# Performance work log

Measured on AMD Instinct MI355X. Metric: run time of the kernel, lower is better.

Reference implementation:

```python
import jax, jax.numpy as jnp
import numpy as np
import itertools

# ---- module hyperparams (from args) ----
B = 4
H, W = 480, 640                 # frame_height, frame_width
NSEM = 16                       # num_sem_categories
RES = 5                         # map_resolution (cm/cell)
ZRES = 5
MAP_CM = 4800 // 2              # map_size_cm // global_downscaling
M = MAP_CM // RES               # local map cells = 480
VR = 100                        # vision_range
FOV = 79.0                      # hfov degrees
DU_SCALE = 1
CAT_THR, EXP_THR, MAP_THR = 5.0, 1.0, 1.0
AGENT_H = 0.88 * 100.0          # camera_height * 100 (cm)
MAX_H = int(360 / ZRES)         # 72
MIN_H = int(-40 / ZRES)         # -8
NZ = MAX_H - MIN_H              # 80 height bins
C = 4 + NSEM                    # obs channels
RAD2DEG = 57.29577951308232


def setup_inputs():
    key = jax.random.key(0)
    k1, k2, k3, k4 = jax.random.split(key, 4)
    obs = jax.random.uniform(k1, (B, C, H, W), dtype=jnp.float32)
    obs = obs.at[:, 3].multiply(500.0)  # depth channel in cm
    pose_obs = jax.random.normal(k2, (B, 3), dtype=jnp.float32) * 0.1
    maps_last = jax.random.uniform(k3, (B, C, M, M), dtype=jnp.float32)
    poses_last = jax.random.normal(k4, (B, 3), dtype=jnp.float32)
    return {"obs": obs, "pose_obs": pose_obs, "maps_last": maps_last, "poses_last": poses_last}


def _point_cloud(depth):
    # du.get_point_cloud_from_z_t; depth: (B,H,W) cm -> (B,H,W,3)
    f = (W / 2.0) / np.tan(np.deg2rad(FOV / 2.0))
    xc, zc = (W - 1) / 2.0, (H - 1) / 2.0
    gx = jnp.arange(W, dtype=jnp.float32)[None, None, :]
    gz = jnp.arange(H - 1, -1, -1, dtype=jnp.float32)[None, :, None]
    X = (gx - xc) * depth / f
    Z = (gz - zc) * depth / f
    return jnp.stack([X, depth, Z], axis=-1)


def _splat_feat_nd(dims, feat, coords):
    # du.splat_feat_nd: trilinear scatter-splat of per-point feats into dense grid.
    # feat: (B,F,N), coords: (B,3,N) normalized to [-1,1]. Returns (B,F,*dims).
    Bn, Fc, N = feat.shape
    pos = [coords[:, d] * (dims[d] / 2.0) + dims[d] / 2.0 for d in range(3)]
    idxs, wtss = [], []
    for offs in itertools.product((0, 1), repeat=3):
        index = jnp.zeros_like(pos[0])
        wts = jnp.ones_like(pos[0])
        for d in range(3):
            p = jnp.floor(pos[d]) + offs[d]
            safe = ((p > 0) & (p < dims[d])).astype(jnp.float32)
            wts = wts * (1.0 - jnp.abs(pos[d] - p)) * safe
            index = index * dims[d] + p * safe
        idxs.append(index)
        wtss.append(wts)
    idx = jnp.concatenate(idxs, -1).astype(jnp.int32)       # (B, 8N)
    wts = jnp.concatenate(wtss, -1)                         # (B, 8N)
    vals = jnp.tile(feat, (1, 1, 8)) * wts[:, None, :]      # (B, F, 8N)
    ncell = dims[0] * dims[1] * dims[2]
    grid = jax.vmap(lambda i, v: jnp.zeros((Fc, ncell), jnp.float32).at[:, i].add(v))(idx, vals)
    return jnp.round(grid).reshape(Bn, Fc, *dims)


def _affine_grid(theta, Hh, Ww):
    # F.affine_grid, align_corners=True. theta: (B,2,3) -> (B,Hh,Ww,2)
    xs = jnp.linspace(-1.0, 1.0, Ww)
    ys = jnp.linspace(-1.0, 1.0, Hh)
    gy, gx = jnp.meshgrid(ys, xs, indexing="ij")
    base = jnp.stack([gx, gy, jnp.ones_like(gx)], -1)       # (Hh,Ww,3)
    return jnp.einsum("hwk,bjk->bhwj", base, theta)


def _grid_sample(img, grid):
    # F.grid_sample bilinear, zeros padding, align_corners=True.
    Bn, Cc, Hi, Wi = img.shape
    x = (grid[..., 0] + 1.0) * 0.5 * (Wi - 1)
    y = (grid[..., 1] + 1.0) * 0.5 * (Hi - 1)
    x0 = jnp.floor(x); y0 = jnp.floor(y)
    x1, y1 = x0 + 1, y0 + 1

    def gather(ix, iy):
        valid = (ix >= 0) & (ix <= Wi - 1) & (iy >= 0) & (iy <= Hi - 1)
        ixc = jnp.clip(ix, 0, Wi - 1).astype(jnp.int32)
        iyc = jnp.clip(iy, 0, Hi - 1).astype(jnp.int32)
        v = jax.vmap(lambda im, yy, xx: im[:, yy, xx])(img, iyc, ixc)  # (B,C,Hg,Wg)
        return v * valid[:, None].astype(img.dtype)

    wa = (x1 - x) * (y1 - y); wb = (x1 - x) * (y - y0)
    wc = (x - x0) * (y1 - y); wd = (x - x0) * (y - y0)
    return (gather(x0, y0) * wa[:, None] + gather(x0, y1) * wb[:, None]
            + gather(x1, y0) * wc[:, None] + gather(x1, y1) * wd[:, None])


def _forward(obs, pose_obs, maps_last, poses_last):
    depth = obs[:, 3]
    pc = _point_cloud(depth)                                # camera frame (cm)
    # transform_camera_view_t with elevation 0 deg: rotation = identity, z += agent height
    av = pc.at[..., 2].add(AGENT_H)
    # transform_pose_t with shift_loc=(vr*res//2, 0, pi/2): rot angle = pi/2-pi/2 = 0, x += shift
    avc = av.at[..., 0].add(VR * RES // 2)
    xy = avc[..., :2] / RES
    xy = (xy - VR // 2.0) / VR * 2.0
    z = avc[..., 2] / ZRES
    z = (z - (MAX_H + MIN_H) // 2.0) / (MAX_H - MIN_H) * 2.0
    coords = jnp.concatenate([xy, z[..., None]], -1)        # (B,H,W,3) in [-1,1]
    coords = coords.reshape(B, H * W, 3).transpose(0, 2, 1)  # (B,3,N)
    # feat: ones occupancy channel + avg-pooled(du_scale) semantic channels
    hs, ws = H // DU_SCALE, W // DU_SCALE
    sem = obs[:, 4:4 + NSEM].reshape(B, NSEM, hs, DU_SCALE, ws, DU_SCALE).mean((3, 5))
    feat = jnp.concatenate([jnp.ones((B, 1, hs * ws), jnp.float32),
                            sem.reshape(B, NSEM, hs * ws)], 1)
    voxels = _splat_feat_nd((VR, VR, NZ), feat, coords)
    voxels = jnp.swapaxes(voxels, 2, 3)                     # .transpose(2, 3)
    min_z = int(25 / ZRES - MIN_H)                          # 13
    max_z = int((AGENT_H + 1) / ZRES - MIN_H)               # 25
    agent_height_proj = voxels[..., min_z:max_z].sum(-1)
    all_height_proj = voxels.sum(-1)
    fp_map_pred = jnp.clip(agent_height_proj[:, 0:1] / MAP_THR, 0.0, 1.0)
    fp_exp_pred = jnp.clip(all_height_proj[:, 0:1] / EXP_THR, 0.0, 1.0)
    agent_view = jnp.zeros((B, C, M, M), jnp.float32)
    x1 = M // 2 - VR // 2; x2 = x1 + VR
    y1 = M // 2; y2 = y1 + VR
    agent_view = agent_view.at[:, 0:1, y1:y2, x1:x2].set(fp_map_pred)
    agent_view = agent_view.at[:, 1:2, y1:y2, x1:x2].set(fp_exp_pred)
    agent_view = agent_view.at[:, 4:, y1:y2, x1:x2].set(
        jnp.clip(agent_height_proj[:, 1:] / CAT_THR, 0.0, 1.0))
    # get_new_pose_batch (uses pre-update theta for x/y, then wraps theta)
    r = poses_last[:, 2] / RAD2DEG
    yy = poses_last[:, 1] + pose_obs[:, 0] * jnp.sin(r) + pose_obs[:, 1] * jnp.cos(r)
    xx = poses_last[:, 0] + pose_obs[:, 0] * jnp.cos(r) - pose_obs[:, 1] * jnp.sin(r)
    oo = poses_last[:, 2] + pose_obs[:, 2] * RAD2DEG
    oo = jnp.fmod(oo - 180.0, 360.0) + 180.0
    oo = jnp.fmod(oo + 180.0, 360.0) - 180.0
    current_poses = jnp.stack([xx, yy, oo], 1)
    st = jax.lax.stop_gradient(current_poses)               # .clone().detach()
    st_xy = -(st[:, :2] * 100.0 / RES - M // 2) / (M // 2)
    st_t = (90.0 - st[:, 2]) * np.pi / 180.0
    cos_t, sin_t = jnp.cos(st_t), jnp.sin(st_t)
    zero = jnp.zeros_like(cos_t); one = jnp.ones_like(cos_t)
    theta1 = jnp.stack([jnp.stack([cos_t, -sin_t, zero], 1),
                        jnp.stack([sin_t, cos_t, zero], 1)], 1)
    theta2 = jnp.stack([jnp.stack([one, zero, st_xy[:, 0]], 1),
                        jnp.stack([zero, one, st_xy[:, 1]], 1)], 1)
    rotated = _grid_sample(agent_view, _affine_grid(theta1, M, M))
    translated = _grid_sample(rotated, _affine_grid(theta2, M, M))
    map_pred = jnp.maximum(maps_last, translated)           # max over stacked maps
    return fp_map_pred, map_pred, current_poses


def reference(obs, pose_obs, maps_last, poses_last):
    return _forward(obs, pose_obs, maps_last, poses_last)
```

## Files before the change

### kernel.cpp

```cpp
#include <hip/hip_runtime.h>
#include <math.h>

#define NB 4
#define NC 20
#define NH 480
#define NW 640
#define NPIX (NH*NW)
#define NM 480
#define NVR 100
#define NNZ 80
#define ZLO 13
#define ZHI 25
#define NZB 12
#define NSEM_ 16
#define NBINS 101

__device__ __forceinline__ float p1_chain(float d) {
  float xy1 = d / 5.0f;
  xy1 = (xy1 - 50.0f) / 100.0f * 2.0f;
  return xy1 * 50.0f + 50.0f;
}
__device__ __forceinline__ void p02_chain(float d, int row, int col, float foc,
                                          float& p0, float& p2) {
  float X = ((float)col - 319.5f) * d / foc;
  float Z = ((float)(479 - row) - 239.5f) * d / foc;
  float xy0 = (X + 250.0f) / 5.0f;
  xy0 = (xy0 - 50.0f) / 100.0f * 2.0f;
  float zz = (Z + 88.0f) / 5.0f;
  zz = (zz - 32.0f) / 80.0f * 2.0f;
  p0 = xy0 * 50.0f + 50.0f;
  p2 = zz * 40.0f + 40.0f;
}

__global__ __launch_bounds__(64) void pose_kernel(
    const float* __restrict__ pose_obs, const float* __restrict__ poses_last,
    float* __restrict__ out_poses, float* __restrict__ params)
{
  int b = threadIdx.x;
  if (b >= NB) return;
  const float R2D = 57.29577951308232f;
  float plx = poses_last[b*3+0], ply = poses_last[b*3+1], plo = poses_last[b*3+2];
  float dx = pose_obs[b*3+0], dy = pose_obs[b*3+1], dth = pose_obs[b*3+2];
  float r = plo / R2D;
  float sr = sinf(r), cr = cosf(r);
  float yy = ply + dx*sr + dy*cr;
  float xx = plx + dx*cr - dy*sr;
  float oo = plo + dth*R2D;
  oo = fmodf(oo - 180.0f, 360.0f) + 180.0f;
  oo = fmodf(oo + 180.0f, 360.0f) - 180.0f;
  out_poses[b*3+0] = xx;
  out_poses[b*3+1] = yy;
  out_poses[b*3+2] = oo;
  float tx = -((xx*100.0f/5.0f) - 240.0f) / 240.0f;
  float ty = -((yy*100.0f/5.0f) - 240.0f) / 240.0f;
  float th = ((90.0f - oo) * 3.14159274101257324f) / 180.0f;
  params[b*4+0] = cosf(th);
  params[b*4+1] = sinf(th);
  params[b*4+2] = tx;
  params[b*4+3] = ty;
}

__global__ __launch_bounds__(256) void hist_kernel(
    const float* __restrict__ obs, int* __restrict__ hist)
{
  int b = blockIdx.x / 300, blk = blockIdx.x % 300;
  __shared__ int lh[NBINS];
  for (int i = threadIdx.x; i < NBINS; i += 256) lh[i] = 0;
  __syncthreads();
  const float4* dp = (const float4*)(obs + ((size_t)b*NC + 3)*NPIX);
  float4 dv = dp[blk*256 + threadIdx.x];
  float dvv[4] = {dv.x, dv.y, dv.z, dv.w};
  #pragma unroll
  for (int k = 0; k < 4; ++k) {
    int y0 = (int)floorf(p1_chain(dvv[k]));
    y0 = min(max(y0, 0), 100);
    atomicAdd(&lh[y0], 1);
  }
  __syncthreads();
  for (int i = threadIdx.x; i < NBINS; i += 256)
    if (lh[i]) atomicAdd(&hist[b*NBINS + i], lh[i]);
}

__global__ __launch_bounds__(512) void scan_kernel(
    const int* __restrict__ hist, int* __restrict__ starts, int* __restrict__ cursors)
{
  __shared__ int lh[NB*NBINS];
  __shared__ int ls[NB*NBINS + 1];
  for (int i = threadIdx.x; i < NB*NBINS; i += 512) lh[i] = hist[i];
  __syncthreads();
  if (threadIdx.x == 0) {
    int s = 0;
    for (int i = 0; i < NB*NBINS; ++i) { ls[i] = s; s += lh[i]; }
    ls[NB*NBINS] = s;
  }
  __syncthreads();
  for (int i = threadIdx.x; i < NB*NBINS + 1; i += 512) {
    starts[i] = ls[i];
    if (i < NB*NBINS) cursors[i] = ls[i];
  }
}

__global__ __launch_bounds__(256) void scatter_kernel(
    const float* __restrict__ obs, int* __restrict__ cursors,
    float4* __restrict__ recs, float foc)
{
  int b = blockIdx.x / 300, blk = blockIdx.x % 300;
  __shared__ int lh[NBINS], lbase[NBINS], loff[NBINS];
  for (int i = threadIdx.x; i < NBINS; i += 256) { lh[i] = 0; loff[i] = 0; }
  __syncthreads();
  int pix0 = (blk*256 + threadIdx.x)*4;
  int row = pix0 / NW;
  int c0 = pix0 - row*NW;
  const float4* dp = (const float4*)(obs + ((size_t)b*NC + 3)*NPIX);
  float4 dv = dp[blk*256 + threadIdx.x];
  float dvv[4] = {dv.x, dv.y, dv.z, dv.w};
  float rp0[4], rp1[4], rp2[4]; int rbin[4];
  #pragma unroll
  for (int k = 0; k < 4; ++k) {
    float p1 = p1_chain(dvv[k]);
    float p0, p2;
    p02_chain(dvv[k], row, c0 + k, foc, p0, p2);
    rp0[k] = p0; rp1[k] = p1; rp2[k] = p2;
    int y0 = (int)floorf(p1); y0 = min(max(y0, 0), 100);
    rbin[k] = y0;
    atomicAdd(&lh[y0], 1);
  }
  __syncthreads();
  for (int i = threadIdx.x; i < NBINS; i += 256)
    if (lh[i] > 0) lbase[i] = atomicAdd(&cursors[b*NBINS + i], lh[i]);
  __syncthreads();
  #pragma unroll
  for (int k = 0; k < 4; ++k) {
    int idx = atomicAdd(&loff[rbin[k]], 1);
    recs[lbase[rbin[k]] + idx] =
        make_float4(rp0[k], rp1[k], rp2[k], __int_as_float(pix0 + k));
  }
}

__global__ __launch_bounds__(256) void slab0_kernel(
    const float4* __restrict__ recs, const int* __restrict__ starts,
    float* __restrict__ proj, float* __restrict__ out_fp)
{
  int b = blockIdx.x / NVR, Y = blockIdx.x % NVR;
  __shared__ float g[NVR*81];
  for (int i = threadIdx.x; i < NVR*81; i += 256) g[i] = 0.0f;
  __syncthreads();
  if (Y > 0) {
    int lo = starts[b*NBINS + Y - 1];
    int hi = starts[b*NBINS + Y + 1];
    float Yf = (float)Y;
    for (int i = lo + threadIdx.x; i < hi; i += 256) {
      float4 r = recs[i];
      float wy = 1.0f - fabsf(r.y - Yf);
      if (wy <= 0.0f) continue;
      float p0 = r.x, p2 = r.z;
      float fl0 = floorf(p0), fl2 = floorf(p2);
      #pragma unroll
      for (int xo = 0; xo < 2; ++xo) {
        float px = fl0 + (float)xo;
        if (!(px > 0.0f && px < 100.0f)) continue;
        float wxy = (1.0f - fabsf(p0 - px)) * wy;
        if (wxy <= 0.0f) continue;
        int ix = (int)px;
        #pragma unroll
        for (int zo = 0; zo < 2; ++zo) {
          float pz = fl2 + (float)zo;
          if (!(pz > 0.0f && pz < 80.0f)) continue;
          float w = wxy * (1.0f - fabsf(p2 - pz));
          if (w > 0.0f) atomicAdd(&g[ix*81 + (int)pz], w);
        }
      }
    }
  }
  __syncthreads();
  if (threadIdx.x < NVR) {
    int x = threadIdx.x;
    float s_all = 0.0f, s_ag = 0.0f;
    for (int z = 0; z < NNZ; ++z) {
      float v = rintf(g[x*81 + z]);
      s_all += v;
      if (z >= ZLO && z < ZHI) s_ag += v;
    }
    float fp_map = fminf(fmaxf(s_ag, 0.0f), 1.0f);
    float fp_exp = fminf(fmaxf(s_all, 0.0f), 1.0f);
    size_t pb = (((size_t)b*NC + 0)*NVR + Y)*NVR + x;
    proj[pb] = fp_map;
    proj[pb + NVR*NVR] = fp_exp;
    proj[pb + 2*NVR*NVR] = 0.0f;
    proj[pb + 3*NVR*NVR] = 0.0f;
    out_fp[(size_t)b*NVR*NVR + Y*NVR + x] = fp_map;
  }
}

__global__ __launch_bounds__(256) void slab1_kernel(
    const float* __restrict__ obs, const float4* __restrict__ recs,
    const int* __restrict__ starts, float* __restrict__ proj)
{
  int half = blockIdx.x & 1;
  int t = blockIdx.x >> 1;
  int b = t / NVR, Y = t % NVR;
  __shared__ float g[NVR*NZB*8];
  for (int i = threadIdx.x; i < NVR*NZB*8; i += 256) g[i] = 0.0f;
  __syncthreads();
  if (Y > 0) {
    int lo = starts[b*NBINS + Y - 1];
    int hi = starts[b*NBINS + Y + 1];
    float Yf = (float)Y;
    const float* sbase = obs + ((size_t)b*NC + 4 + half*8)*NPIX;
    for (int i = lo + threadIdx.x; i < hi; i += 256) {
      float4 r = recs[i];
      float wy = 1.0f - fabsf(r.y - Yf);
      if (wy <= 0.0f) continue;
      float p2 = r.z;
      float fl2 = floorf(p2);
      float wz[2]; int iz[2]; bool any = false;
      #pragma unroll
      for (int zo = 0; zo < 2; ++zo) {
        float pz = fl2 + (float)zo;
        bool v = (pz >= (float)ZLO) && (pz < (float)ZHI);
        float w = v ? (1.0f - fabsf(p2 - pz)) : 0.0f;
        wz[zo] = w; iz[zo] = v ? ((int)pz - ZLO) : 0;
        any = any || (w > 0.0f);
      }
      if (!any) continue;
      float p0 = r.x;
      float fl0 = floorf(p0);
      int pid = __float_as_int(r.w);
      float sem[8];
      #pragma unroll
      for (int s = 0; s < 8; ++s) sem[s] = sbase[(size_t)s*NPIX + pid];
      #pragma unroll
      for (int xo = 0; xo < 2; ++xo) {
        float px = fl0 + (float)xo;
        if (!(px > 0.0f && px < 100.0f)) continue;
        float wxy = (1.0f - fabsf(p0 - px)) * wy;
        if (wxy <= 0.0f) continue;
        int ix = (int)px;
        #pragma unroll
        for (int zo = 0; zo < 2; ++zo) {
          float w = wxy * wz[zo];
          if (w > 0.0f) {
            float* gb = &g[(ix*NZB + iz[zo])*8];
            #pragma unroll
            for (int s = 0; s < 8; ++s) atomicAdd(&gb[s], w * sem[s]);
          }
        }
      }
    }
  }
  __syncthreads();
  for (int p = threadIdx.x; p < NVR*8; p += 256) {
    int x = p >> 3, s = p & 7;
    float acc = 0.0f;
    #pragma unroll
    for (int z = 0; z < NZB; ++z) acc += rintf(g[(x*NZB + z)*8 + s]);
    float val = fminf(fmaxf(acc / 5.0f, 0.0f), 1.0f);
    proj[(((size_t)b*NC + 4 + half*8 + s)*NVR + Y)*NVR + x] = val;
  }
}

__global__ __launch_bounds__(256) void transform_kernel(
    const float* __restrict__ maps_last, const float* __restrict__ proj,
    const float* __restrict__ params, float* __restrict__ d_out)
{
  int tid = blockIdx.x * 256 + threadIdx.x;
  int b = tid / (NM*NM);
  int rem = tid - b*(NM*NM);
  int h = rem / NM;
  int w = rem - h*NM;

  float ct = params[b*4+0];
  float st = params[b*4+1];
  float tx = params[b*4+2];
  float ty = params[b*4+3];

  const float step = 2.0f/479.0f;
  float gx = -1.0f + (float)w * step;
  float gy = -1.0f + (float)h * step;
  float X2 = ((gx + tx) + 1.0f) * 0.5f * 479.0f;
  float Y2 = ((gy + ty) + 1.0f) * 0.5f * 479.0f;
  float x0 = floorf(X2), y0 = floorf(Y2);
  float wox[2] = {(x0 + 1.0f) - X2, X2 - x0};
  float woy[2] = {(y0 + 1.0f) - Y2, Y2 - y0};

  float twt[16];
  int   toff[16];
  int nz = 0;
  #pragma unroll
  for (int oy = 0; oy < 2; ++oy) {
    #pragma unroll
    for (int ox = 0; ox < 2; ++ox) {
      int kb = (oy*2 + ox)*4;
      float cx = x0 + (float)ox;
      float cy = y0 + (float)oy;
      float wo = wox[ox]*woy[oy];
      bool ov = (cx >= 0.0f) && (cx <= 479.0f) && (cy >= 0.0f) && (cy <= 479.0f);
      if (ov) {
        float gxr = -1.0f + cx * step;
        float gyr = -1.0f + cy * step;
        float xr = gxr*ct - gyr*st;
        float yr = gxr*st + gyr*ct;
        float XS = (xr + 1.0f)*0.5f*479.0f;
        float YS = (yr + 1.0f)*0.5f*479.0f;
        float ix0 = floorf(XS), iy0 = floorf(YS);
        float wix[2] = {(ix0+1.0f)-XS, XS-ix0};
        float wiy[2] = {(iy0+1.0f)-YS, YS-iy0};
        #pragma unroll
        for (int qy = 0; qy < 2; ++qy) {
          #pragma unroll
          for (int qx = 0; qx < 2; ++qx) {
            int k = kb + qy*2 + qx;
            float ux = ix0 + (float)qx;
            float vy = iy0 + (float)qy;
            float wv = 0.0f; int off = 0;
            if (ux >= 0.0f && ux <= 479.0f && vy >= 0.0f && vy <= 479.0f) {
              int U = (int)ux, V = (int)vy;
              if (U >= 190 && U < 290 && V >= 240 && V < 340) {
                off = (V - 240)*NVR + (U - 190);
                wv = wo * (wix[qx]*wiy[qy]);
              }
            }
            twt[k] = wv; toff[k] = off;
            nz += (wv != 0.0f) ? 1 : 0;
          }
        }
      } else {
        #pragma unroll
        for (int k = 0; k < 4; ++k) { twt[kb+k] = 0.0f; toff[kb+k] = 0; }
      }
    }
  }

  const float* pbase = proj + (size_t)b*NC*NVR*NVR;
  size_t base_idx = (size_t)b*NC*NM*NM + (size_t)h*NM + w;
  if (nz > 0) {
    #pragma unroll 1
    for (int c = 0; c < NC; ++c) {
      size_t idx = base_idx + (size_t)c*NM*NM;
      float ml = maps_last[idx];
      float val = 0.0f;
      if (c != 2 && c != 3) {
        const float* pc = pbase + (size_t)c*NVR*NVR;
        #pragma unroll
        for (int k = 0; k < 16; ++k) val += twt[k]*pc[toff[k]];
      }
      d_out[40000 + idx] = fmaxf(ml, val);
    }
  } else {
    #pragma unroll 1
    for (int c = 0; c < NC; ++c) {
      size_t idx = base_idx + (size_t)c*NM*NM;
      d_out[40000 + idx] = fmaxf(maps_last[idx], 0.0f);
    }
  }
}

extern "C" void kernel_launch(void* const* d_in, const int* in_sizes, int n_in,
                              void* d_out, int out_size, void* d_ws, size_t ws_size,
                              hipStream_t stream)
{
  const float* obs        = (const float*)d_in[0];
  const float* pose_obs   = (const float*)d_in[1];
  const float* maps_last  = (const float*)d_in[2];
  const float* poses_last = (const float*)d_in[3];
  float* out = (float*)d_out;

  char* ws = (char*)d_ws;
  int*    hist    = (int*)ws;
  int*    starts  = (int*)(ws + 2048);
  int*    cursors = (int*)(ws + 4096);
  float*  params  = (float*)(ws + 6144);
  float4* recs    = (float4*)(ws + 8192);
  float*  proj    = (float*)(ws + 8192 + 19660800);

  hipMemsetAsync(ws, 0, 6144, stream);

  const float foc = (float)(((double)NW) / 2.0 / tan(79.0 * 0.5 * M_PI / 180.0));

  pose_kernel<<<1, 64, 0, stream>>>(pose_obs, poses_last, out + 40000 + 18432000, params);
  hist_kernel<<<NB*300, 256, 0, stream>>>(obs, hist);
  scan_kernel<<<1, 512, 0, stream>>>(hist, starts, cursors);
  scatter_kernel<<<NB*300, 256, 0, stream>>>(obs, cursors, recs, foc);
  slab0_kernel<<<NB*NVR, 256, 0, stream>>>(recs, starts, proj, out);
  slab1_kernel<<<NB*NVR*2, 256, 0, stream>>>(obs, recs, starts, proj);
  transform_kernel<<<(NB*NM*NM)/256, 256, 0, stream>>>(maps_last, proj, params, out);
}
```

Before: 560.5 us.

## Compact band-filtered points with semantic features for coalesced semantic splatting

Adds a second histogram and scan that count only points whose x and z fall inside the agent-height band, then has the scatter kernel write those points' geometry and all 16 semantic values contiguously into compact buffers. A new slab1f kernel reads these packed records instead of gathering semantic channels from obs by pixel index, so it skips out-of-band points and avoids scattered loads. The fast path runs only when the workspace is large enough. In exchange, hist and scatter do more arithmetic, scatter reads extra channels and writes more, and anything beyond SREC_CAP is silently dropped.

```diff
diff --git a/kernel.cpp b/kernel.cpp
--- a/kernel.cpp
+++ b/kernel.cpp
@@ -14,6 +14,20 @@
 #define NZB 12
 #define NSEM_ 16
 #define NBINS 101
+#define SREC_CAP 655360
+
+#define WS_HIST     0
+#define WS_HIST2    2048
+#define WS_STARTS   4096
+#define WS_STARTS2  6144
+#define WS_CURS     8192
+#define WS_CURS2    10240
+#define WS_PARAMS   12288
+#define WS_RECS     16384
+#define WS_PROJ     (WS_RECS + 19660800)
+#define WS_SGEOM    (WS_PROJ + 3200000)
+#define WS_SSEM     (WS_SGEOM + SREC_CAP*16)
+#define WS_FAST_END (WS_SSEM + (size_t)SREC_CAP*64)
 
 __device__ __forceinline__ float p1_chain(float d) {
   float xy1 = d / 5.0f;
@@ -30,6 +44,10 @@
   zz = (zz - 32.0f) / 80.0f * 2.0f;
   p0 = xy0 * 50.0f + 50.0f;
   p2 = zz * 40.0f + 40.0f;
+}
+__device__ __forceinline__ bool band_ok(float p0, float p2) {
+  return (p0 > 0.0f) && (p0 < 100.0f) &&
+         (p2 > (float)(ZLO - 1)) && (p2 < (float)ZHI);
 }
 
 __global__ __launch_bounds__(64) void pose_kernel(
@@ -61,52 +79,12 @@
 }
 
 __global__ __launch_bounds__(256) void hist_kernel(
-    const float* __restrict__ obs, int* __restrict__ hist)
+    const float* __restrict__ obs, int* __restrict__ hist, int* __restrict__ hist2,
+    float foc)
 {
   int b = blockIdx.x / 300, blk = blockIdx.x % 300;
-  __shared__ int lh[NBINS];
-  for (int i = threadIdx.x; i < NBINS; i += 256) lh[i] = 0;
-  __syncthreads();
-  const float4* dp = (const float4*)(obs + ((size_t)b*NC + 3)*NPIX);
-  float4 dv = dp[blk*256 + threadIdx.x];
-  float dvv[4] = {dv.x, dv.y, dv.z, dv.w};
-  #pragma unroll
-  for (int k = 0; k < 4; ++k) {
-    int y0 = (int)floorf(p1_chain(dvv[k]));
-    y0 = min(max(y0, 0), 100);
-    atomicAdd(&lh[y0], 1);
-  }
-  __syncthreads();
-  for (int i = threadIdx.x; i < NBINS; i += 256)
-    if (lh[i]) atomicAdd(&hist[b*NBINS + i], lh[i]);
-}
-
-__global__ __launch_bounds__(512) void scan_kernel(
-    const int* __restrict__ hist, int* __restrict__ starts, int* __restrict__ cursors)
-{
-  __shared__ int lh[NB*NBINS];
-  __shared__ int ls[NB*NBINS + 1];
-  for (int i = threadIdx.x; i < NB*NBINS; i += 512) lh[i] = hist[i];
-  __syncthreads();
-  if (threadIdx.x == 0) {
-    int s = 0;
-    for (int i = 0; i < NB*NBINS; ++i) { ls[i] = s; s += lh[i]; }
-    ls[NB*NBINS] = s;
-  }
-  __syncthreads();
-  for (int i = threadIdx.x; i < NB*NBINS + 1; i += 512) {
-    starts[i] = ls[i];
-    if (i < NB*NBINS) cursors[i] = ls[i];
-  }
-}
-
-__global__ __launch_bounds__(256) void scatter_kernel(
-    const float* __restrict__ obs, int* __restrict__ cursors,
-    float4* __restrict__ recs, float foc)
-{
-  int b = blockIdx.x / 300, blk = blockIdx.x % 300;
-  __shared__ int lh[NBINS], lbase[NBINS], loff[NBINS];
-  for (int i = threadIdx.x; i < NBINS; i += 256) { lh[i] = 0; loff[i] = 0; }
+  __shared__ int lh[NBINS], lh2[NBINS];
+  for (int i = threadIdx.x; i < NBINS; i += 256) { lh[i] = 0; lh2[i] = 0; }
   __syncthreads();
   int pix0 = (blk*256 + threadIdx.x)*4;
   int row = pix0 / NW;
@@ -114,7 +92,69 @@
   const float4* dp = (const float4*)(obs + ((size_t)b*NC + 3)*NPIX);
   float4 dv = dp[blk*256 + threadIdx.x];
   float dvv[4] = {dv.x, dv.y, dv.z, dv.w};
-  float rp0[4], rp1[4], rp2[4]; int rbin[4];
+  #pragma unroll
+  for (int k = 0; k < 4; ++k) {
+    float p1 = p1_chain(dvv[k]);
+    int y0 = (int)floorf(p1);
+    y0 = min(max(y0, 0), 100);
+    atomicAdd(&lh[y0], 1);
+    float p0, p2;
+    p02_chain(dvv[k], row, c0 + k, foc, p0, p2);
+    if (band_ok(p0, p2)) atomicAdd(&lh2[y0], 1);
+  }
+  __syncthreads();
+  for (int i = threadIdx.x; i < NBINS; i += 256) {
+    if (lh[i])  atomicAdd(&hist[b*NBINS + i],  lh[i]);
+    if (lh2[i]) atomicAdd(&hist2[b*NBINS + i], lh2[i]);
+  }
+}
+
+__global__ __launch_bounds__(512) void scan_kernel(
+    const int* __restrict__ hist, const int* __restrict__ hist2,
+    int* __restrict__ starts, int* __restrict__ cursors,
+    int* __restrict__ starts2, int* __restrict__ cursors2)
+{
+  __shared__ int lh[NB*NBINS], lh2[NB*NBINS];
+  __shared__ int ls[NB*NBINS + 1], ls2[NB*NBINS + 1];
+  for (int i = threadIdx.x; i < NB*NBINS; i += 512) { lh[i] = hist[i]; lh2[i] = hist2[i]; }
+  __syncthreads();
+  if (threadIdx.x == 0) {
+    int s = 0;
+    for (int i = 0; i < NB*NBINS; ++i) { ls[i] = s; s += lh[i]; }
+    ls[NB*NBINS] = s;
+  }
+  if (threadIdx.x == 1) {
+    int s = 0;
+    for (int i = 0; i < NB*NBINS; ++i) { ls2[i] = s; s += lh2[i]; }
+    ls2[NB*NBINS] = s;
+  }
+  __syncthreads();
+  for (int i = threadIdx.x; i < NB*NBINS + 1; i += 512) {
+    starts[i] = ls[i];
+    starts2[i] = ls2[i];
+    if (i < NB*NBINS) { cursors[i] = ls[i]; cursors2[i] = ls2[i]; }
+  }
+}
+
+__global__ __launch_bounds__(256) void scatter_kernel(
+    const float* __restrict__ obs, int* __restrict__ cursors, int* __restrict__ cursors2,
+    float4* __restrict__ recs, float4* __restrict__ sgeom, float4* __restrict__ ssem,
+    float foc, int do_band)
+{
+  int b = blockIdx.x / 300, blk = blockIdx.x % 300;
+  __shared__ int lh[NBINS], lbase[NBINS], loff[NBINS];
+  __shared__ int lh2[NBINS], lbase2[NBINS], loff2[NBINS];
+  for (int i = threadIdx.x; i < NBINS; i += 256) {
+    lh[i] = 0; loff[i] = 0; lh2[i] = 0; loff2[i] = 0;
+  }
+  __syncthreads();
+  int pix0 = (blk*256 + threadIdx.x)*4;
+  int row = pix0 / NW;
+  int c0 = pix0 - row*NW;
+  const float4* dp = (const float4*)(obs + ((size_t)b*NC + 3)*NPIX);
+  float4 dv = dp[blk*256 + threadIdx.x];
+  float dvv[4] = {dv.x, dv.y, dv.z, dv.w};
+  float rp0[4], rp1[4], rp2[4]; int rbin[4]; bool rb[4];
   #pragma unroll
   for (int k = 0; k < 4; ++k) {
     float p1 = p1_chain(dvv[k]);
@@ -124,16 +164,50 @@
     int y0 = (int)floorf(p1); y0 = min(max(y0, 0), 100);
     rbin[k] = y0;
     atomicAdd(&lh[y0], 1);
-  }
-  __syncthreads();
-  for (int i = threadIdx.x; i < NBINS; i += 256)
-    if (lh[i] > 0) lbase[i] = atomicAdd(&cursors[b*NBINS + i], lh[i]);
-  __syncthreads();
+    rb[k] = do_band && band_ok(p0, p2);
+    if (rb[k]) atomicAdd(&lh2[y0], 1);
+  }
+  __syncthreads();
+  for (int i = threadIdx.x; i < NBINS; i += 256) {
+    if (lh[i]  > 0) lbase[i]  = atomicAdd(&cursors[b*NBINS + i],  lh[i]);
+    if (lh2[i] > 0) lbase2[i] = atomicAdd(&cursors2[b*NBINS + i], lh2[i]);
+  }
+  __syncthreads();
+  int sidx[4];
   #pragma unroll
   for (int k = 0; k < 4; ++k) {
     int idx = atomicAdd(&loff[rbin[k]], 1);
     recs[lbase[rbin[k]] + idx] =
         make_float4(rp0[k], rp1[k], rp2[k], __int_as_float(pix0 + k));
+    sidx[k] = -1;
+    if (rb[k]) {
+      int j = lbase2[rbin[k]] + atomicAdd(&loff2[rbin[k]], 1);
+      if (j < SREC_CAP) sidx[k] = j;
+    }
+  }
+  bool anyb = (sidx[0] >= 0) | (sidx[1] >= 0) | (sidx[2] >= 0) | (sidx[3] >= 0);
+  if (anyb) {
+    #pragma unroll
+    for (int k = 0; k < 4; ++k)
+      if (sidx[k] >= 0)
+        sgeom[sidx[k]] = make_float4(rp0[k], rp1[k], rp2[k], 0.0f);
+    int grp = blk*256 + threadIdx.x;
+    const float4* obs4 = (const float4*)obs;
+    #pragma unroll
+    for (int q = 0; q < 4; ++q) {
+      float4 v0 = obs4[(((size_t)b*NC + 4 + 4*q + 0)*NPIX >> 2) + grp];
+      float4 v1 = obs4[(((size_t)b*NC + 4 + 4*q + 1)*NPIX >> 2) + grp];
+      float4 v2 = obs4[(((size_t)b*NC + 4 + 4*q + 2)*NPIX >> 2) + grp];
+      float4 v3 = obs4[(((size_t)b*NC + 4 + 4*q + 3)*NPIX >> 2) + grp];
+      float a0[4] = {v0.x, v0.y, v0.z, v0.w};
+      float a1[4] = {v1.x, v1.y, v1.z, v1.w};
+      float a2[4] = {v2.x, v2.y, v2.z, v2.w};
+      float a3[4] = {v3.x, v3.y, v3.z, v3.w};
+      #pragma unroll
+      for (int k = 0; k < 4; ++k)
+        if (sidx[k] >= 0)
+          ssem[(size_t)sidx[k]*4 + q] = make_float4(a0[k], a1[k], a2[k], a3[k]);
+    }
   }
 }
 
@@ -189,6 +263,72 @@
     proj[pb + 2*NVR*NVR] = 0.0f;
     proj[pb + 3*NVR*NVR] = 0.0f;
     out_fp[(size_t)b*NVR*NVR + Y*NVR + x] = fp_map;
+  }
+}
+
+__global__ __launch_bounds__(256) void slab1f_kernel(
+    const float4* __restrict__ sgeom, const float4* __restrict__ ssem,
+    const int* __restrict__ starts2, float* __restrict__ proj)
+{
+  int half = blockIdx.x & 1;
+  int t = blockIdx.x >> 1;
+  int b = t / NVR, Y = t % NVR;
+  __shared__ float g[8*NVR*NZB];
+  for (int i = threadIdx.x; i < 8*NVR*NZB; i += 256) g[i] = 0.0f;
+  __syncthreads();
+  if (Y > 0) {
+    int lo = starts2[b*NBINS + Y - 1];
+    int hi = starts2[b*NBINS + Y + 1];
+    float Yf = (float)Y;
+    for (int i = lo + threadIdx.x; i < hi; i += 256) {
+      float4 ge = sgeom[i];
+      float wy = 1.0f - fabsf(ge.y - Yf);
+      if (wy <= 0.0f) continue;
+      float p2 = ge.z;
+      float fl2 = floorf(p2);
+      float wz[2]; int iz[2]; bool any = false;
+      #pragma unroll
+      for (int zo = 0; zo < 2; ++zo) {
+        float pz = fl2 + (float)zo;
+        bool v = (pz >= (float)ZLO) && (pz < (float)ZHI);
+        float w = v ? (1.0f - fabsf(p2 - pz)) : 0.0f;
+        wz[zo] = w; iz[zo] = v ? ((int)pz - ZLO) : 0;
+        any = any || (w > 0.0f);
+      }
+      if (!any) continue;
+      float p0 = ge.x;
+      float fl0 = floorf(p0);
+      float4 s0 = ssem[(size_t)i*4 + half*2];
+      float4 s1 = ssem[(size_t)i*4 + half*2 + 1];
+      float sem[8] = {s0.x, s0.y, s0.z, s0.w, s1.x, s1.y, s1.z, s1.w};
+      #pragma unroll
+      for (int xo = 0; xo < 2; ++xo) {
+        float px = fl0 + (float)xo;
+        if (!(px > 0.0f && px < 100.0f)) continue;
+        float wxy = (1.0f - fabsf(p0 - px)) * wy;
+        if (wxy <= 0.0f) continue;
+        int ix = (int)px;
+        #pragma unroll
+        for (int zo = 0; zo < 2; ++zo) {
+          float w = wxy * wz[zo];
+          if (w > 0.0f) {
+            int cell = ix*NZB + iz[zo];
+            #pragma unroll
+            for (int s = 0; s < 8; ++s)
+              atomicAdd(&g[s*(NVR*NZB) + cell], w * sem[s]);
+          }
+        }
+      }
+    }
+  }
+  __syncthreads();
+  for (int p = threadIdx.x; p < NVR*8; p += 256) {
+    int x = p >> 3, s = p & 7;
+    float acc = 0.0f;
+    #pragma unroll
+    for (int z = 0; z < NZB; ++z) acc += rintf(g[s*(NVR*NZB) + x*NZB + z]);
+    float val = fminf(fmaxf(acc / 5.0f, 0.0f), 1.0f);
+    proj[(((size_t)b*NC + 4 + half*8 + s)*NVR + Y)*NVR + x] = val;
   }
 }
 
@@ -366,22 +506,33 @@
   float* out = (float*)d_out;
 
   char* ws = (char*)d_ws;
-  int*    hist    = (int*)ws;
-  int*    starts  = (int*)(ws + 2048);
-  int*    cursors = (int*)(ws + 4096);
-  float*  params  = (float*)(ws + 6144);
-  float4* recs    = (float4*)(ws + 8192);
-  float*  proj    = (float*)(ws + 8192 + 19660800);
-
-  hipMemsetAsync(ws, 0, 6144, stream);
+  int*    hist    = (int*)(ws + WS_HIST);
+  int*    hist2   = (int*)(ws + WS_HIST2);
+  int*    starts  = (int*)(ws + WS_STARTS);
+  int*    starts2 = (int*)(ws + WS_STARTS2);
+  int*    cursors = (int*)(ws + WS_CURS);
+  int*    cursors2= (int*)(ws + WS_CURS2);
+  float*  params  = (float*)(ws + WS_PARAMS);
+  float4* recs    = (float4*)(ws + WS_RECS);
+  float*  proj    = (float*)(ws + WS_PROJ);
+  float4* sgeom   = (float4*)(ws + WS_SGEOM);
+  float4* ssem    = (float4*)(ws + WS_SSEM);
+
+  const bool fast = ws_size >= (size_t)WS_FAST_END;
+
+  hipMemsetAsync(ws, 0, WS_PARAMS, stream);
 
   const float foc = (float)(((double)NW) / 2.0 / tan(79.0 * 0.5 * M_PI / 180.0));
 
   pose_kernel<<<1, 64, 0, stream>>>(pose_obs, poses_last, out + 40000 + 18432000, params);
-  hist_kernel<<<NB*300, 256, 0, stream>>>(obs, hist);
-  scan_kernel<<<1, 512, 0, stream>>>(hist, starts, cursors);
-  scatter_kernel<<<NB*300, 256, 0, stream>>>(obs, cursors, recs, foc);
+  hist_kernel<<<NB*300, 256, 0, stream>>>(obs, hist, hist2, foc);
+  scan_kernel<<<1, 512, 0, stream>>>(hist, hist2, starts, cursors, starts2, cursors2);
+  scatter_kernel<<<NB*300, 256, 0, stream>>>(obs, cursors, cursors2, recs, sgeom, ssem,
+                                             foc, fast ? 1 : 0);
   slab0_kernel<<<NB*NVR, 256, 0, stream>>>(recs, starts, proj, out);
-  slab1_kernel<<<NB*NVR*2, 256, 0, stream>>>(obs, recs, starts, proj);
+  if (fast)
+    slab1f_kernel<<<NB*NVR*2, 256, 0, stream>>>(sgeom, ssem, starts2, proj);
+  else
+    slab1_kernel<<<NB*NVR*2, 256, 0, stream>>>(obs, recs, starts, proj);
   transform_kernel<<<(NB*NM*NM)/256, 256, 0, stream>>>(maps_last, proj, params, out);
 }
```

Result: slower. 603.6 us (+7.7%).

## Bin semantic splat by (Y,X) cells and gather-accumulate from transposed semantics

Applied to the files above, without the earlier changes.

Adds a 2D (Y,X) histogram and scan so that only points inside the agent-height band are scattered into per-cell record lists. A transpose kernel lays the 16 semantic channels out per pixel, and a new gather kernel has lanes accumulate per-cell sums in registers, replacing the shared-memory atomic splat. The slab0 loop is also unrolled to load four records at a time. The gain depends on the band filter pruning most points. The cost is an extra full semantic transpose pass, more workspace, and a fallback path when the workspace is too small.

```diff
diff --git a/kernel.cpp b/kernel.cpp
--- a/kernel.cpp
+++ b/kernel.cpp
@@ -12,8 +12,22 @@
 #define ZLO 13
 #define ZHI 25
 #define NZB 12
-#define NSEM_ 16
 #define NBINS 101
+#define SREC_CAP 786432
+#define NB2D 40400
+
+#define WS_HIST     0
+#define WS_STARTS   2048
+#define WS_CURS     4096
+#define WS_PARAMS   6144
+#define WS_H2D      8192
+#define WS_S2D      172032
+#define WS_C2D      335872
+#define WS_RECS     499712
+#define WS_PROJ     (WS_RECS + 19660800)
+#define WS_SGEOM    (WS_PROJ + 3200000)
+#define WS_SEMT     (WS_SGEOM + (size_t)SREC_CAP*16)
+#define WS_FAST_END (WS_SEMT + (size_t)NB*NPIX*16*4)
 
 __device__ __forceinline__ float p1_chain(float d) {
   float xy1 = d / 5.0f;
@@ -30,6 +44,10 @@
   zz = (zz - 32.0f) / 80.0f * 2.0f;
   p0 = xy0 * 50.0f + 50.0f;
   p2 = zz * 40.0f + 40.0f;
+}
+__device__ __forceinline__ bool band_ok(float p0, float p2) {
+  return (p0 > 0.0f) && (p0 < 100.0f) &&
+         (p2 > (float)(ZLO - 1)) && (p2 < (float)ZHI);
 }
 
 __global__ __launch_bounds__(64) void pose_kernel(
@@ -60,21 +78,48 @@
   params[b*4+3] = ty;
 }
 
+__global__ __launch_bounds__(256) void semt_kernel(
+    const float* __restrict__ obs, float* __restrict__ semT)
+{
+  int b = blockIdx.x / 1200, blk = blockIdx.x % 1200;
+  int p = blk*256 + threadIdx.x;
+  const float* src = obs + ((size_t)b*NC + 4)*NPIX + p;
+  float v[16];
+  #pragma unroll
+  for (int s = 0; s < 16; ++s) v[s] = src[(size_t)s*NPIX];
+  float4* dst = (float4*)(semT + ((size_t)b*NPIX + p)*16);
+  dst[0] = make_float4(v[0],  v[1],  v[2],  v[3]);
+  dst[1] = make_float4(v[4],  v[5],  v[6],  v[7]);
+  dst[2] = make_float4(v[8],  v[9],  v[10], v[11]);
+  dst[3] = make_float4(v[12], v[13], v[14], v[15]);
+}
+
 __global__ __launch_bounds__(256) void hist_kernel(
-    const float* __restrict__ obs, int* __restrict__ hist)
+    const float* __restrict__ obs, int* __restrict__ hist, int* __restrict__ h2d,
+    float foc, int do2d)
 {
   int b = blockIdx.x / 300, blk = blockIdx.x % 300;
   __shared__ int lh[NBINS];
   for (int i = threadIdx.x; i < NBINS; i += 256) lh[i] = 0;
   __syncthreads();
+  int pix0 = (blk*256 + threadIdx.x)*4;
+  int row = pix0 / NW;
+  int c0 = pix0 - row*NW;
   const float4* dp = (const float4*)(obs + ((size_t)b*NC + 3)*NPIX);
   float4 dv = dp[blk*256 + threadIdx.x];
   float dvv[4] = {dv.x, dv.y, dv.z, dv.w};
   #pragma unroll
   for (int k = 0; k < 4; ++k) {
-    int y0 = (int)floorf(p1_chain(dvv[k]));
+    float p1 = p1_chain(dvv[k]);
+    int y0 = (int)floorf(p1);
     y0 = min(max(y0, 0), 100);
     atomicAdd(&lh[y0], 1);
+    float p0, p2;
+    p02_chain(dvv[k], row, c0 + k, foc, p0, p2);
+    if (do2d && band_ok(p0, p2)) {
+      int x0 = (int)floorf(p0);
+      atomicAdd(&h2d[(b*NBINS + y0)*100 + x0], 1);
+    }
   }
   __syncthreads();
   for (int i = threadIdx.x; i < NBINS; i += 256)
@@ -100,9 +145,37 @@
   }
 }
 
+__global__ __launch_bounds__(512) void scan2d_kernel(
+    const int* __restrict__ h2d, int* __restrict__ s2d, int* __restrict__ c2d)
+{
+  __shared__ int part[512];
+  __shared__ int base[512];
+  const int CH = 79;
+  int t = threadIdx.x;
+  int s = 0;
+  for (int i = 0; i < CH; ++i) {
+    int idx = t*CH + i;
+    if (idx < NB2D) s += h2d[idx];
+  }
+  part[t] = s;
+  __syncthreads();
+  if (t == 0) {
+    int run = 0;
+    for (int k = 0; k < 512; ++k) { base[k] = run; run += part[k]; }
+    s2d[NB2D] = run;
+  }
+  __syncthreads();
+  int run = base[t];
+  for (int i = 0; i < CH; ++i) {
+    int idx = t*CH + i;
+    if (idx < NB2D) { s2d[idx] = run; c2d[idx] = run; run += h2d[idx]; }
+  }
+}
+
 __global__ __launch_bounds__(256) void scatter_kernel(
-    const float* __restrict__ obs, int* __restrict__ cursors,
-    float4* __restrict__ recs, float foc)
+    const float* __restrict__ obs, int* __restrict__ cursors, int* __restrict__ c2d,
+    float4* __restrict__ recs, float4* __restrict__ sgeom,
+    float foc, int do_band)
 {
   int b = blockIdx.x / 300, blk = blockIdx.x % 300;
   __shared__ int lh[NBINS], lbase[NBINS], loff[NBINS];
@@ -134,10 +207,17 @@
     int idx = atomicAdd(&loff[rbin[k]], 1);
     recs[lbase[rbin[k]] + idx] =
         make_float4(rp0[k], rp1[k], rp2[k], __int_as_float(pix0 + k));
-  }
-}
-
-__global__ __launch_bounds__(256) void slab0_kernel(
+    if (do_band && band_ok(rp0[k], rp2[k])) {
+      int x0 = (int)floorf(rp0[k]);
+      int bin = (b*NBINS + rbin[k])*100 + x0;
+      int j = atomicAdd(&c2d[bin], 1);
+      if (j < SREC_CAP)
+        sgeom[j] = make_float4(rp0[k], rp1[k], rp2[k], __int_as_float(pix0 + k));
+    }
+  }
+}
+
+__global__ __launch_bounds__(256) void slab0f_kernel(
     const float4* __restrict__ recs, const int* __restrict__ starts,
     float* __restrict__ proj, float* __restrict__ out_fp)
 {
@@ -149,25 +229,34 @@
     int lo = starts[b*NBINS + Y - 1];
     int hi = starts[b*NBINS + Y + 1];
     float Yf = (float)Y;
-    for (int i = lo + threadIdx.x; i < hi; i += 256) {
-      float4 r = recs[i];
-      float wy = 1.0f - fabsf(r.y - Yf);
-      if (wy <= 0.0f) continue;
-      float p0 = r.x, p2 = r.z;
-      float fl0 = floorf(p0), fl2 = floorf(p2);
+    for (int i = lo + threadIdx.x; i < hi; i += 1024) {
+      float4 rr[4];
       #pragma unroll
-      for (int xo = 0; xo < 2; ++xo) {
-        float px = fl0 + (float)xo;
-        if (!(px > 0.0f && px < 100.0f)) continue;
-        float wxy = (1.0f - fabsf(p0 - px)) * wy;
-        if (wxy <= 0.0f) continue;
-        int ix = (int)px;
+      for (int k = 0; k < 4; ++k) {
+        int j = i + k*256;
+        rr[k] = (j < hi) ? recs[j] : make_float4(0.0f, -1.0e9f, 0.0f, 0.0f);
+      }
+      #pragma unroll
+      for (int k = 0; k < 4; ++k) {
+        float4 r = rr[k];
+        float wy = 1.0f - fabsf(r.y - Yf);
+        if (wy <= 0.0f) continue;
+        float p0 = r.x, p2 = r.z;
+        float fl0 = floorf(p0), fl2 = floorf(p2);
         #pragma unroll
-        for (int zo = 0; zo < 2; ++zo) {
-          float pz = fl2 + (float)zo;
-          if (!(pz > 0.0f && pz < 80.0f)) continue;
-          float w = wxy * (1.0f - fabsf(p2 - pz));
-          if (w > 0.0f) atomicAdd(&g[ix*81 + (int)pz], w);
+        for (int xo = 0; xo < 2; ++xo) {
+          float px = fl0 + (float)xo;
+          if (!(px > 0.0f && px < 100.0f)) continue;
+          float wxy = (1.0f - fabsf(p0 - px)) * wy;
+          if (wxy <= 0.0f) continue;
+          int ix = (int)px;
+          #pragma unroll
+          for (int zo = 0; zo < 2; ++zo) {
+            float pz = fl2 + (float)zo;
+            if (!(pz > 0.0f && pz < 80.0f)) continue;
+            float w = wxy * (1.0f - fabsf(p2 - pz));
+            if (w > 0.0f) atomicAdd(&g[ix*81 + (int)pz], w);
+          }
         }
       }
     }
@@ -189,6 +278,69 @@
     proj[pb + 2*NVR*NVR] = 0.0f;
     proj[pb + 3*NVR*NVR] = 0.0f;
     out_fp[(size_t)b*NVR*NVR + Y*NVR + x] = fp_map;
+  }
+}
+
+__global__ __launch_bounds__(512) void slab1g_kernel(
+    const float* __restrict__ semT, const float4* __restrict__ sgeom,
+    const int* __restrict__ s2d, float* __restrict__ proj)
+{
+  int b = blockIdx.x / NVR, Y = blockIdx.x % NVR;
+  int wave = threadIdx.x >> 6;
+  int lane = threadIdx.x & 63;
+  int s = lane & 15;
+  int zq = lane >> 4;
+  float z0f = (float)(ZLO + zq*3);
+  float Yf = (float)Y;
+  const float* sT = semT + (size_t)b*NPIX*16 + s;
+
+  int xbase = wave*13;
+  #pragma unroll 1
+  for (int xi = 0; xi < 13; ++xi) {
+    int x = xbase + xi;
+    if (x >= NVR) break;
+    float acc0 = 0.0f, acc1 = 0.0f, acc2 = 0.0f;
+    if (Y > 0 && x > 0) {
+      float xf = (float)x;
+      #pragma unroll 1
+      for (int p = 0; p < 2; ++p) {
+        int rowb = (b*NBINS + (Y - 1 + p))*100;
+        int lo = s2d[rowb + x - 1];
+        int hi = s2d[rowb + x + 1];
+        #pragma unroll 1
+        for (int i = lo; i < hi; i += 4) {
+          int n = hi - i;
+          float4 gm[4];
+          #pragma unroll
+          for (int k = 0; k < 4; ++k)
+            gm[k] = (k < n) ? sgeom[i + k]
+                            : make_float4(0.0f, -1.0e9f, 0.0f, __int_as_float(0));
+          float sv[4];
+          #pragma unroll
+          for (int k = 0; k < 4; ++k) {
+            int pid = __float_as_int(gm[k].w);
+            sv[k] = sT[(size_t)pid*16];
+          }
+          #pragma unroll
+          for (int k = 0; k < 4; ++k) {
+            float wy = fmaxf(1.0f - fabsf(gm[k].y - Yf), 0.0f);
+            float wx = fmaxf(1.0f - fabsf(gm[k].x - xf), 0.0f);
+            float wxy = wx * wy;
+            float p2 = gm[k].z;
+            float ws0 = wxy * sv[k];
+            acc0 += ws0 * fmaxf(1.0f - fabsf(p2 - z0f), 0.0f);
+            acc1 += ws0 * fmaxf(1.0f - fabsf(p2 - (z0f + 1.0f)), 0.0f);
+            acc2 += ws0 * fmaxf(1.0f - fabsf(p2 - (z0f + 2.0f)), 0.0f);
+          }
+        }
+      }
+    }
+    float r = rintf(acc0) + rintf(acc1) + rintf(acc2);
+    r += __shfl_xor(r, 16);
+    r += __shfl_xor(r, 32);
+    if (zq == 0)
+      proj[(((size_t)b*NC + 4 + s)*NVR + Y)*NVR + x] =
+          fminf(fmaxf(r / 5.0f, 0.0f), 1.0f);
   }
 }
 
@@ -228,7 +380,7 @@
       int pid = __float_as_int(r.w);
       float sem[8];
       #pragma unroll
-      for (int s = 0; s < 8; ++s) sem[s] = sbase[(size_t)s*NPIX + pid];
+      for (int ss = 0; ss < 8; ++ss) sem[ss] = sbase[(size_t)ss*NPIX + pid];
       #pragma unroll
       for (int xo = 0; xo < 2; ++xo) {
         float px = fl0 + (float)xo;
@@ -242,7 +394,7 @@
           if (w > 0.0f) {
             float* gb = &g[(ix*NZB + iz[zo])*8];
             #pragma unroll
-            for (int s = 0; s < 8; ++s) atomicAdd(&gb[s], w * sem[s]);
+            for (int ss = 0; ss < 8; ++ss) atomicAdd(&gb[ss], w * sem[ss]);
           }
         }
       }
@@ -250,12 +402,12 @@
   }
   __syncthreads();
   for (int p = threadIdx.x; p < NVR*8; p += 256) {
-    int x = p >> 3, s = p & 7;
+    int x = p >> 3, ss = p & 7;
     float acc = 0.0f;
     #pragma unroll
-    for (int z = 0; z < NZB; ++z) acc += rintf(g[(x*NZB + z)*8 + s]);
+    for (int z = 0; z < NZB; ++z) acc += rintf(g[(x*NZB + z)*8 + ss]);
     float val = fminf(fmaxf(acc / 5.0f, 0.0f), 1.0f);
-    proj[(((size_t)b*NC + 4 + half*8 + s)*NVR + Y)*NVR + x] = val;
+    proj[(((size_t)b*NC + 4 + half*8 + ss)*NVR + Y)*NVR + x] = val;
   }
 }
 
@@ -366,22 +518,37 @@
   float* out = (float*)d_out;
 
   char* ws = (char*)d_ws;
-  int*    hist    = (int*)ws;
-  int*    starts  = (int*)(ws + 2048);
-  int*    cursors = (int*)(ws + 4096);
-  float*  params  = (float*)(ws + 6144);
-  float4* recs    = (float4*)(ws + 8192);
-  float*  proj    = (float*)(ws + 8192 + 19660800);
-
-  hipMemsetAsync(ws, 0, 6144, stream);
+  int*    hist    = (int*)(ws + WS_HIST);
+  int*    starts  = (int*)(ws + WS_STARTS);
+  int*    cursors = (int*)(ws + WS_CURS);
+  float*  params  = (float*)(ws + WS_PARAMS);
+  int*    h2d     = (int*)(ws + WS_H2D);
+  int*    s2d     = (int*)(ws + WS_S2D);
+  int*    c2d     = (int*)(ws + WS_C2D);
+  float4* recs    = (float4*)(ws + WS_RECS);
+  float*  proj    = (float*)(ws + WS_PROJ);
+  float4* sgeom   = (float4*)(ws + WS_SGEOM);
+  float*  semT    = (float*)(ws + WS_SEMT);
+
+  const bool fast = ws_size >= (size_t)WS_FAST_END;
+
+  hipMemsetAsync(ws, 0, WS_S2D, stream);
 
   const float foc = (float)(((double)NW) / 2.0 / tan(79.0 * 0.5 * M_PI / 180.0));
 
   pose_kernel<<<1, 64, 0, stream>>>(pose_obs, poses_last, out + 40000 + 18432000, params);
-  hist_kernel<<<NB*300, 256, 0, stream>>>(obs, hist);
+  if (fast)
+    semt_kernel<<<NB*1200, 256, 0, stream>>>(obs, semT);
+  hist_kernel<<<NB*300, 256, 0, stream>>>(obs, hist, h2d, foc, fast ? 1 : 0);
   scan_kernel<<<1, 512, 0, stream>>>(hist, starts, cursors);
-  scatter_kernel<<<NB*300, 256, 0, stream>>>(obs, cursors, recs, foc);
-  slab0_kernel<<<NB*NVR, 256, 0, stream>>>(recs, starts, proj, out);
-  slab1_kernel<<<NB*NVR*2, 256, 0, stream>>>(obs, recs, starts, proj);
+  if (fast)
+    scan2d_kernel<<<1, 512, 0, stream>>>(h2d, s2d, c2d);
+  scatter_kernel<<<NB*300, 256, 0, stream>>>(obs, cursors, c2d, recs, sgeom,
+                                             foc, fast ? 1 : 0);
+  slab0f_kernel<<<NB*NVR, 256, 0, stream>>>(recs, starts, proj, out);
+  if (fast)
+    slab1g_kernel<<<NB*NVR, 512, 0, stream>>>(semT, sgeom, s2d, proj);
+  else
+    slab1_kernel<<<NB*NVR*2, 256, 0, stream>>>(obs, recs, starts, proj);
   transform_kernel<<<(NB*NM*NM)/256, 256, 0, stream>>>(maps_last, proj, params, out);
 }
```

Result: slower. 1.145 ms (+104.3%).
